# Performance work log

Measured on AMD Instinct MI355X. Metric: run time of the kernel, lower is better.

The kernel has to match this reference:

```python
import jax, jax.numpy as jnp
import numpy as np
import math

WINDOW = 14
NUM_HEADS = 12


def setup_inputs() -> dict:
    key = jax.random.key(0)
    k1, k2, k3 = jax.random.split(key, 3)
    B, H, W, C = 8, 80, 80, 768
    x = jax.random.normal(k1, (B, H * W, C), dtype=jnp.float32)
    Wqkv = jax.random.normal(k2, (C, 3 * C), dtype=jnp.float32) * 0.02
    Wproj = jax.random.normal(k3, (C, C), dtype=jnp.float32) * 0.02
    bproj = jnp.zeros((C,), dtype=jnp.float32)
    return {"x": x, "Wqkv": Wqkv, "Wproj": Wproj, "bproj": bproj, "H": H, "W": W}


def reference(x, Wqkv, Wproj, bproj, H, W):
    B, N, C = x.shape
    w = WINDOW
    nh = NUM_HEADS
    hd = C // nh
    scale = hd ** (-0.5)
    Hp = math.ceil(H / w) * w
    Wp = math.ceil(W / w) * w
    nH, nW = Hp // w, Wp // w
    L, Nw = nH * nW, w * w

    qkv = x @ Wqkv                                   # [B, N, 3C]
    grid = qkv.reshape(B, H, W, 3 * C)
    grid = jnp.pad(grid, ((0, 0), (0, Hp - H), (0, Wp - W), (0, 0)))
    # window partition: [B, nH, w, nW, w, 3C] -> [B, L, Nw, 3, nh, hd]
    win = grid.reshape(B, nH, w, nW, w, 3 * C).transpose(0, 1, 3, 2, 4, 5)
    win = win.reshape(B, L, Nw, 3, nh, hd)
    q = win[:, :, :, 0].transpose(0, 1, 3, 2, 4)     # [B, L, nh, Nw, hd]
    k = win[:, :, :, 1].transpose(0, 1, 3, 2, 4)
    v = win[:, :, :, 2].transpose(0, 1, 3, 2, 4)

    attn = jnp.einsum('blhnd,blhmd->blhnm', q, k) * scale
    attn = jax.nn.softmax(attn, axis=-1)
    out = jnp.einsum('blhnm,blhmd->blhnd', attn, v)  # [B, L, nh, Nw, hd]

    # window merge (fold with stride == kernel, non-overlapping)
    out = out.transpose(0, 1, 3, 2, 4).reshape(B, nH, nW, w, w, C)
    out = out.transpose(0, 1, 3, 2, 4, 5).reshape(B, Hp, Wp, C)
    out = out[:, :H, :W, :].reshape(B, N, C)
    return out @ Wproj + bproj
```

## Files before the change

kernel.cpp:

```cpp
#include <hip/hip_runtime.h>

typedef unsigned short u16;
typedef __attribute__((ext_vector_type(4))) float f32x4;
typedef __attribute__((ext_vector_type(8))) short bf16x8;

__device__ __forceinline__ u16 f2bf(float f) {
  unsigned u = __builtin_bit_cast(unsigned, f);
  u += 0x7FFFu + ((u >> 16) & 1u);
  return (u16)(u >> 16);
}

__device__ __forceinline__ void load16(const void* g, void* l) {
  __builtin_amdgcn_global_load_lds((const __attribute__((address_space(1))) void*)g,
                                   (__attribute__((address_space(3))) void*)l, 16, 0, 0);
}

#define LDS_ORDER() do { __builtin_amdgcn_s_waitcnt(0xC07F); asm volatile("" ::: "memory"); } while (0)

#define FENCE() asm volatile("" ::: "memory")
#define BARRIER() do { FENCE(); __builtin_amdgcn_s_barrier(); FENCE(); } while (0)
#define WAIT_VM2() asm volatile("s_waitcnt vmcnt(2)" ::: "memory")
#define WAIT_VM0() asm volatile("s_waitcnt vmcnt(0)" ::: "memory")
#define LGKM0() asm volatile("s_waitcnt lgkmcnt(0)" ::: "memory")


__global__ void cvt_x(const float* __restrict__ in, u16* __restrict__ out, int n4) {
  int i = blockIdx.x * 256 + threadIdx.x;
  if (i < n4) {
    float4 v = ((const float4*)in)[i];
    ushort4 o;
    o.x = f2bf(v.x); o.y = f2bf(v.y); o.z = f2bf(v.z); o.w = f2bf(v.w);
    ((ushort4*)out)[i] = o;
  }
}

__global__ void cvt_wt(const float* __restrict__ W, u16* __restrict__ Wt, int K, int N) {
  int idx = blockIdx.x * 256 + threadIdx.x;
  if (idx < N * K) {
    int n = idx / K, k = idx - n * K;
    Wt[idx] = f2bf(W[(size_t)k * N + n]);
  }
}


template <int MB, int NB>
__device__ __forceinline__ void mfma_quad(f32x4 (&acc)[8][4], const bf16x8 (&af)[4][2],
                                          const bf16x8 (&bf_)[4][2]) {
  __builtin_amdgcn_s_setprio(1);
#pragma unroll
  for (int mf = 0; mf < 4; mf++)
#pragma unroll
    for (int nf = 0; nf < 2; nf++) {
      acc[MB + mf][NB + nf] = __builtin_amdgcn_mfma_f32_16x16x32_bf16(
          af[mf][0], bf_[NB + nf][0], acc[MB + mf][NB + nf], 0, 0, 0);
      acc[MB + mf][NB + nf] = __builtin_amdgcn_mfma_f32_16x16x32_bf16(
          af[mf][1], bf_[NB + nf][1], acc[MB + mf][NB + nf], 0, 0, 0);
    }
  __builtin_amdgcn_s_setprio(0);
}

__device__ __forceinline__ void mm256_core(const u16* __restrict__ A,
                                           const u16* __restrict__ Bt,
                                           int bm, int bn,
                                           u16* lds, f32x4 (&acc)[8][4]) {
  const int K = 768;
  const int t = threadIdx.x;
  const int lane = t & 63, wave = t >> 6;
  const int wm = wave >> 2, wn = wave & 3;
  const int colq = lane & 15, quad = lane >> 4;

  const u16* Ab = A + (size_t)bm * 256 * K;
  const u16* Bb = Bt + (size_t)bn * 256 * K;

  u16* const lA = lds;
  u16* const lB = lds + 32768;

  const int srow = t >> 3;
  const int gslot = (t & 7) ^ (srow & 7);

#define STAGE_(gb, lb)                                                          \
  do {                                                                          \
    load16((gb) + (size_t)srow * K + gslot * 8, (lb) + t * 8);                  \
    load16((gb) + (size_t)(srow + 64) * K + gslot * 8, (lb) + (t + 512) * 8);   \
  } while (0)
#define STAGE_A(jj, h) STAGE_(Ab + (size_t)((h) * 128) * K + (jj) * 64, \
                              lA + ((jj) & 1) * 16384 + (h) * 8192)
#define STAGE_B(jj, h) STAGE_(Bb + (size_t)((h) * 128) * K + (jj) * 64, \
                              lB + ((jj) & 1) * 16384 + (h) * 8192)

  const int arow_lo = wm * 128 + colq;
  const int brow_lo = wn * 64 + colq;
  const int swz = (colq & 7) << 3;
#define RD(buf, row, kk) (*(const bf16x8*)&(buf)[(row) * 64 + (((kk) * 32 + quad * 8) ^ swz)])

  bf16x8 af[4][2], bf_[4][2];

  STAGE_A(0, 0); STAGE_A(0, 1); STAGE_B(0, 0); STAGE_B(0, 1);
  STAGE_A(1, 0);
  WAIT_VM2();
  BARRIER();

#pragma unroll 2
  for (int j = 0; j < 12; ++j) {
    const u16* cA = lA + (j & 1) * 16384;
    const u16* cB = lB + (j & 1) * 16384;

#pragma unroll
    for (int mf = 0; mf < 4; mf++) {
      af[mf][0] = RD(cA, arow_lo + mf * 16, 0);
      af[mf][1] = RD(cA, arow_lo + mf * 16, 1);
    }
#pragma unroll
    for (int nf = 0; nf < 2; nf++) {
      bf_[nf][0] = RD(cB, brow_lo + nf * 16, 0);
      bf_[nf][1] = RD(cB, brow_lo + nf * 16, 1);
    }
    if (j < 11) STAGE_A(j + 1, 1);
    BARRIER();
    mfma_quad<0, 0>(acc, af, bf_);
    LGKM0();
    BARRIER();

#pragma unroll
    for (int nf = 0; nf < 2; nf++) {
      bf_[2 + nf][0] = RD(cB, brow_lo + (2 + nf) * 16, 0);
      bf_[2 + nf][1] = RD(cB, brow_lo + (2 + nf) * 16, 1);
    }
    if (j < 11) STAGE_B(j + 1, 0);
    BARRIER();
    mfma_quad<0, 2>(acc, af, bf_);
    LGKM0();
    BARRIER();

#pragma unroll
    for (int mf = 0; mf < 4; mf++) {
      af[mf][0] = RD(cA, arow_lo + 64 + mf * 16, 0);
      af[mf][1] = RD(cA, arow_lo + 64 + mf * 16, 1);
    }
    if (j < 11) STAGE_B(j + 1, 1);
    BARRIER();
    mfma_quad<4, 0>(acc, af, bf_);
    LGKM0();
    BARRIER();

    if (j < 10) STAGE_A(j + 2, 0);
    BARRIER();
    mfma_quad<4, 2>(acc, af, bf_);
    if (j < 10) { WAIT_VM2(); }
    else if (j < 11) { WAIT_VM0(); }
    BARRIER();
  }
#undef RD
#undef STAGE_A
#undef STAGE_B
#undef STAGE_
}


__global__ __launch_bounds__(512, 2) void gemm_qkv(const u16* __restrict__ A,
                                                   const u16* __restrict__ Bt,
                                                   u16* __restrict__ qkvP) {
  __shared__ __align__(16) u16 lds[65536];
  const int nx = gridDim.x;
  const int nwg = nx * gridDim.y;
  const int bid = blockIdx.y * nx + blockIdx.x;
  const int cpx = nwg >> 3;
  const int sid = (bid & 7) * cpx + (bid >> 3);
  const int bm = sid / nx, bn = sid - bm * nx;

  f32x4 acc[8][4] = {};
  mm256_core(A, Bt, bm, bn, lds, acc);

  const int t = threadIdx.x;
  const int lane = t & 63, wave = t >> 6;
  const int wm = wave >> 2, wn = wave & 3;
  const int colq = lane & 15, quad = lane >> 4;

  const int c64 = bn * 4 + wn;
  const int mat = c64 / 12;
  const int hh = c64 - mat * 12;
  const int r0 = bm * 256 + wm * 128 + quad * 4;
#pragma unroll
  for (int mf = 0; mf < 8; mf++) {
#pragma unroll
    for (int r = 0; r < 4; r++) {
      int row = r0 + mf * 16 + r;
      int bb = row / 6400;
      int rem = row - bb * 6400;
      int y = rem / 80, x = rem - (rem / 80) * 80;
      int wy = y / 14, wx = x / 14;
      int iy = y - wy * 14, ix = x - wx * 14;
      int win = wy * 6 + wx;
      int kidx = iy * 14 + ix;
      size_t base = ((size_t)((bb * 36 + win) * 3 + mat) * 12 + hh) * 12544 + (size_t)kidx * 64;
#pragma unroll
      for (int nf = 0; nf < 4; nf++)
        qkvP[base + nf * 16 + colq] = f2bf(acc[mf][nf][r]);
    }
  }
}


__global__ __launch_bounds__(512, 2) void gemm_proj(const u16* __restrict__ A,
                                                    const u16* __restrict__ Bt,
                                                    float* __restrict__ C,
                                                    const float* __restrict__ bias) {
  __shared__ __align__(16) u16 lds[65536];
  const int nx = gridDim.x;
  const int nwg = nx * gridDim.y;
  const int bid = blockIdx.y * nx + blockIdx.x;
  const int cpx = nwg >> 3;
  const int sid = (bid & 7) * cpx + (bid >> 3);
  const int bm = sid / nx, bn = sid - bm * nx;

  f32x4 acc[8][4] = {};
  mm256_core(A, Bt, bm, bn, lds, acc);

  const int t = threadIdx.x;
  const int lane = t & 63, wave = t >> 6;
  const int wm = wave >> 2, wn = wave & 3;
  const int colq = lane & 15, quad = lane >> 4;

  const int r0 = bm * 256 + wm * 128 + quad * 4;
  const int c0 = bn * 256 + wn * 64 + colq;
  float bv[4];
#pragma unroll
  for (int nf = 0; nf < 4; nf++) bv[nf] = bias[c0 + nf * 16];
#pragma unroll
  for (int mf = 0; mf < 8; mf++)
#pragma unroll
    for (int nf = 0; nf < 4; nf++)
#pragma unroll
      for (int r = 0; r < 4; r++)
        C[(size_t)(r0 + mf * 16 + r) * 768 + (c0 + nf * 16)] = acc[mf][nf][r] + bv[nf];
}


__global__ __launch_bounds__(256) void win_attn(const u16* __restrict__ qkvP,
                                                u16* __restrict__ out) {
  __shared__ __align__(16) u16 sK[2 * 208 * 32];
  __shared__ __align__(16) u16 sVt[7 * 64 * 32];
  __shared__ __align__(16) u16 sVrow[200 * 64];

  const int h = blockIdx.x;
  const int win = blockIdx.y;
  const int b = blockIdx.z;
  const int wy = win / 6, wx = win - wy * 6;
  const int y0 = wy * 14, x0 = wx * 14;
  const int t = threadIdx.x, wave = t >> 6, lane = t & 63;
  const int colq = lane & 15, quad = lane >> 4;

  const size_t bwin = (size_t)(b * 36 + win) * 3;
  const u16* qbase = qkvP + ((bwin + 0) * 12 + h) * 12544;
  const u16* kbase = qkvP + ((bwin + 1) * 12 + h) * 12544;
  const u16* vbase = qkvP + ((bwin + 2) * 12 + h) * 12544;

  for (int s = t; s < 3264; s += 256) {
    if (s < 1664) {
      int half = s / 832;
      int rem = s - half * 832;
      int row = rem >> 2, e = rem & 3;
      int srow = row < 196 ? row : 0;
      load16(kbase + srow * 64 + half * 32 + e * 8, (u16*)sK + s * 8);
    } else {
      int s2 = s - 1664;
      load16(vbase + s2 * 8, sVrow + s2 * 8);
    }
  }
  __syncthreads();

  const bool boundary = (wx == 5) || (wy == 5);
  for (int jj = t; jj < 14336; jj += 256) {
    int kc = jj >> 11;
    int r2 = jj & 2047;
    int j = r2 >> 6, d = r2 & 63;
    int k = (j + d) & 31;
    int kidx = kc * 32 + k;
    u16 val = 0;
    if (kidx < 196) {
      int iy = kidx / 14, ix = kidx - (kidx / 14) * 14;
      if (y0 + iy < 80 && x0 + ix < 80) val = sVrow[kidx * 64 + d];
    }
    sVt[kc * 2048 + d * 32 + k] = val;
  }
  if (boundary) {
    for (int jj = t; jj < 13312; jj += 256) {
      int row = jj >> 6, d = jj & 63;
      if (row < 196) {
        int iy = row / 14, ix = row - (row / 14) * 14;
        if (y0 + iy >= 80 || x0 + ix >= 80)
          sK[((d >> 5) * 208 + row) * 32 + (d & 31)] = 0;
      }
    }
  }
  __syncthreads();

  u16* sPw = sVrow + wave * 640;

  int mt = wave;
  const u16* qp = qbase + (mt * 16 + colq) * 64 + quad * 8;
  bf16x8 qa0 = *(const bf16x8*)qp;
  bf16x8 qa1 = *(const bf16x8*)(qp + 32);
  while (mt < 13) {
    int mtn = mt + 4;
    bf16x8 qn0 = qa0, qn1 = qa1;
    if (mtn < 13) {
      const u16* qp2 = qbase + (mtn * 16 + colq) * 64 + quad * 8;
      qn0 = *(const bf16x8*)qp2;
      qn1 = *(const bf16x8*)(qp2 + 32);
    }

    f32x4 s[13];
#pragma unroll
    for (int nt = 0; nt < 13; nt++) {
      bf16x8 kb0 = *(const bf16x8*)&sK[(nt * 16 + colq) * 32 + quad * 8];
      bf16x8 kb1 = *(const bf16x8*)&sK[((208 + nt * 16 + colq)) * 32 + quad * 8];
      f32x4 a = {0.f, 0.f, 0.f, 0.f};
      a = __builtin_amdgcn_mfma_f32_16x16x32_bf16(qa0, kb0, a, 0, 0, 0);
      a = __builtin_amdgcn_mfma_f32_16x16x32_bf16(qa1, kb1, a, 0, 0, 0);
      s[nt] = a;
    }

    float mx[4] = {-1e30f, -1e30f, -1e30f, -1e30f};
#pragma unroll
    for (int nt = 0; nt < 13; nt++)
#pragma unroll
      for (int r = 0; r < 4; r++) {
        float v = s[nt][r] * 0.125f;
        if (nt == 12 && colq >= 4) v = -1e30f;
        s[nt][r] = v;
        mx[r] = fmaxf(mx[r], v);
      }
#pragma unroll
    for (int off = 1; off < 16; off <<= 1)
#pragma unroll
      for (int r = 0; r < 4; r++) mx[r] = fmaxf(mx[r], __shfl_xor(mx[r], off));
    float sm[4] = {0.f, 0.f, 0.f, 0.f};
#pragma unroll
    for (int nt = 0; nt < 13; nt++)
#pragma unroll
      for (int r = 0; r < 4; r++) {
        float e = __expf(s[nt][r] - mx[r]);
        s[nt][r] = e;
        sm[r] += e;
      }
#pragma unroll
    for (int off = 1; off < 16; off <<= 1)
#pragma unroll
      for (int r = 0; r < 4; r++) sm[r] += __shfl_xor(sm[r], off);
    float rs[4];
#pragma unroll
    for (int r = 0; r < 4; r++) rs[r] = 1.0f / sm[r];

    f32x4 o[4] = {};
#pragma unroll
    for (int kc = 0; kc < 7; kc++) {
      const int nt0 = kc * 2, nt1 = kc * 2 + 1;
#pragma unroll
      for (int r = 0; r < 4; r++) {
        sPw[(quad * 4 + r) * 36 + colq] = f2bf(s[nt0][r] * rs[r]);
        sPw[(quad * 4 + r) * 36 + 16 + colq] = (nt1 < 13) ? f2bf(s[nt1][r] * rs[r]) : (u16)0;
      }
      LDS_ORDER();
      bf16x8 pa = *(const bf16x8*)&sPw[colq * 36 + quad * 8];
#pragma unroll
      for (int dt = 0; dt < 4; dt++) {
        bf16x8 vb = *(const bf16x8*)&sVt[(kc * 64 + dt * 16 + colq) * 32 + quad * 8];
        o[dt] = __builtin_amdgcn_mfma_f32_16x16x32_bf16(pa, vb, o[dt], 0, 0, 0);
      }
      LDS_ORDER();
    }

#pragma unroll
    for (int r = 0; r < 4; r++) {
      int qr = mt * 16 + quad * 4 + r;
      if (qr < 196) {
        int iy = qr / 14, ix = qr - (qr / 14) * 14;
        int y = y0 + iy, x = x0 + ix;
        if (y < 80 && x < 80) {
          size_t off = ((size_t)(b * 6400 + y * 80 + x)) * 768 + h * 64 + colq;
#pragma unroll
          for (int dt = 0; dt < 4; dt++) out[off + dt * 16] = f2bf(o[dt][r]);
        }
      }
    }
    qa0 = qn0; qa1 = qn1;
    mt = mtn;
  }
}


extern "C" void kernel_launch(void* const* d_in, const int* in_sizes, int n_in,
                              void* d_out, int out_size, void* d_ws, size_t ws_size,
                              hipStream_t stream) {
  const float* x     = (const float*)d_in[0];
  const float* Wqkv  = (const float*)d_in[1];
  const float* Wproj = (const float*)d_in[2];
  const float* bproj = (const float*)d_in[3];

  char* ws = (char*)d_ws;
  const size_t QKVP_BYTES = (size_t)130056192 * 2 + 4096;
  const size_t X_BYTES    = (size_t)51200 * 768 * 2;
  const size_t WQT_BYTES  = (size_t)2304 * 768 * 2;
  u16* qkvP   = (u16*)ws;
  u16* xbf    = (u16*)(ws + QKVP_BYTES);
  u16* wqkvT  = (u16*)(ws + QKVP_BYTES + X_BYTES);
  u16* wprojT = (u16*)(ws + QKVP_BYTES + X_BYTES + WQT_BYTES);
  u16* aout   = xbf;

  cvt_x<<<38400, 256, 0, stream>>>(x, xbf, 9830400);
  cvt_wt<<<6912, 256, 0, stream>>>(Wqkv, wqkvT, 768, 2304);
  cvt_wt<<<2304, 256, 0, stream>>>(Wproj, wprojT, 768, 768);
  gemm_qkv<<<dim3(9, 200), 512, 0, stream>>>(xbf, wqkvT, qkvP);
  win_attn<<<dim3(12, 36, 8), 256, 0, stream>>>(qkvP, aout);
  gemm_proj<<<dim3(3, 200), 512, 0, stream>>>(aout, wprojT, (float*)d_out, bproj);
}
```

Measured before the change: 779.6 us.

## Keep softmax probabilities in registers and swizzle K/V LDS layouts in window attention

The window attention kernel now computes the score tile with K as the A operand, so each lane holds one query column. That lets the softmax reductions shrink to two cross-lane shuffles, and the normalised probabilities are packed straight into bf16 registers as the MFMA A operand, removing the per-chunk LDS round trip and its waits. K is loaded with an XOR swizzle, and V is transposed on load from global with byte permutes into a swizzled layout, replacing the staging buffer and second transpose pass. Zeroing of padded K/V rows moves into a separate pre-pass kernel on the workspace, and the kernel asks for 3 blocks per CU. The risks are the extra launch and the reliance on the QKV GEMM never overwriting the padded rows.

Result: faster. 749.2 us (-3.9%).

```diff
diff --git a/kernel.cpp b/kernel.cpp
--- a/kernel.cpp
+++ b/kernel.cpp
@@ -3,6 +3,12 @@
 typedef unsigned short u16;
 typedef __attribute__((ext_vector_type(4))) float f32x4;
 typedef __attribute__((ext_vector_type(8))) short bf16x8;
+typedef __attribute__((ext_vector_type(4))) short bf16x4;
+typedef __attribute__((ext_vector_type(2))) unsigned uint32x2;
+
+#ifndef __has_builtin
+#define __has_builtin(x) 0
+#endif
 
 __device__ __forceinline__ u16 f2bf(float f) {
   unsigned u = __builtin_bit_cast(unsigned, f);
@@ -15,7 +21,22 @@
                                    (__attribute__((address_space(3))) void*)l, 16, 0, 0);
 }
 
-#define LDS_ORDER() do { __builtin_amdgcn_s_waitcnt(0xC07F); asm volatile("" ::: "memory"); } while (0)
+__device__ __forceinline__ unsigned cvt_pk_bf16(float lo, float hi) {
+  unsigned r;
+  asm("v_cvt_pk_bf16_f32 %0, %1, %2" : "=v"(r) : "v"(lo), "v"(hi));
+  return r;
+}
+
+__device__ __forceinline__ f32x4 mfma16_bf16(bf16x4 a, bf16x4 b, f32x4 c) {
+#if __has_builtin(__builtin_amdgcn_mfma_f32_16x16x16bf16_1k)
+  return __builtin_amdgcn_mfma_f32_16x16x16bf16_1k(a, b, c, 0, 0, 0);
+#else
+  f32x4 d;
+  asm volatile("v_mfma_f32_16x16x16_bf16 %0, %1, %2, %3\n\ts_nop 7\n\ts_nop 3"
+               : "=&v"(d) : "v"(a), "v"(b), "v"(c));
+  return d;
+#endif
+}
 
 #define FENCE() asm volatile("" ::: "memory")
 #define BARRIER() do { FENCE(); __builtin_amdgcn_s_barrier(); FENCE(); } while (0)
@@ -40,6 +61,22 @@
     int n = idx / K, k = idx - n * K;
     Wt[idx] = f2bf(W[(size_t)k * N + n]);
   }
+}
+
+__global__ void zero_pad(u16* __restrict__ qkvP) {
+  int tid = blockIdx.x * 256 + threadIdx.x;
+  if (tid >= 1354752) return;
+  int kidx = tid % 196; int t2 = tid / 196;
+  int h = t2 % 12;      int t3 = t2 / 12;
+  int matp = t3 % 2;    int t4 = t3 / 2;
+  int win = t4 % 36;    int b = t4 / 36;
+  int wy = win / 6, wx = win - wy * 6;
+  int iy = kidx / 14, ix = kidx - iy * 14;
+  if (wy * 14 + iy < 80 && wx * 14 + ix < 80) return;
+  size_t base = ((size_t)((b * 36 + win) * 3 + (matp + 1)) * 12 + h) * 12544 + (size_t)kidx * 64;
+  f32x4 z = {};
+#pragma unroll
+  for (int i = 0; i < 8; i++) ((f32x4*)(qkvP + base))[i] = z;
 }
 
 
@@ -236,15 +273,12 @@
 }
 
 
-__global__ __launch_bounds__(256) void win_attn(const u16* __restrict__ qkvP,
-                                                u16* __restrict__ out) {
-  __shared__ __align__(16) u16 sK[2 * 208 * 32];
-  __shared__ __align__(16) u16 sVt[7 * 64 * 32];
-  __shared__ __align__(16) u16 sVrow[200 * 64];
-
-  const int h = blockIdx.x;
-  const int win = blockIdx.y;
-  const int b = blockIdx.z;
+__global__ __launch_bounds__(256, 3) void win_attn(const u16* __restrict__ qkvP,
+                                                   u16* __restrict__ out) {
+  __shared__ __align__(16) u16 sK[208 * 64];
+  __shared__ __align__(16) u16 sVt[13 * 1024];
+
+  const int h = blockIdx.x, win = blockIdx.y, b = blockIdx.z;
   const int wy = win / 6, wx = win - wy * 6;
   const int y0 = wy * 14, x0 = wx * 14;
   const int t = threadIdx.x, wave = t >> 6, lane = t & 63;
@@ -255,47 +289,39 @@
   const u16* kbase = qkvP + ((bwin + 1) * 12 + h) * 12544;
   const u16* vbase = qkvP + ((bwin + 2) * 12 + h) * 12544;
 
-  for (int s = t; s < 3264; s += 256) {
-    if (s < 1664) {
-      int half = s / 832;
-      int rem = s - half * 832;
-      int row = rem >> 2, e = rem & 3;
-      int srow = row < 196 ? row : 0;
-      load16(kbase + srow * 64 + half * 32 + e * 8, (u16*)sK + s * 8);
-    } else {
-      int s2 = s - 1664;
-      load16(vbase + s2 * 8, sVrow + s2 * 8);
+  for (int s = t; s < 1664; s += 256) {
+    int row = s >> 3, g = s & 7;
+    int srow = row < 196 ? row : 0;
+    load16(kbase + srow * 64 + ((g ^ (row & 7)) << 3), (u16*)sK + s * 8);
+  }
+
+  for (int u = t; u < 416; u += 256) {
+    int kq = u >> 3, dg = u & 7;
+    int nt = kq >> 2, q = kq & 3;
+    uint4 a0 = {}, a1 = {}, a2 = {}, a3 = {};
+    if (kq < 49) {
+      const uint4* vp = (const uint4*)(vbase + kq * 256 + dg * 8);
+      a0 = vp[0]; a1 = vp[8]; a2 = vp[16]; a3 = vp[24];
+    }
+    const unsigned* r0p = (const unsigned*)&a0;
+    const unsigned* r1p = (const unsigned*)&a1;
+    const unsigned* r2p = (const unsigned*)&a2;
+    const unsigned* r3p = (const unsigned*)&a3;
+#pragma unroll
+    for (int dd = 0; dd < 8; dd++) {
+      unsigned sel = (dd & 1) ? 0x07060302u : 0x05040100u;
+      unsigned lo = __builtin_amdgcn_perm(r1p[dd >> 1], r0p[dd >> 1], sel);
+      unsigned hi = __builtin_amdgcn_perm(r3p[dd >> 1], r2p[dd >> 1], sel);
+      int byteoff = nt * 2048 + (dg >> 1) * 512 + q * 128 +
+                    ((((dg & 1) * 8 + dd) ^ (q << 2)) << 3);
+      uint32x2 wv; wv[0] = lo; wv[1] = hi;
+      *(uint32x2*)((char*)sVt + byteoff) = wv;
     }
   }
   __syncthreads();
 
-  const bool boundary = (wx == 5) || (wy == 5);
-  for (int jj = t; jj < 14336; jj += 256) {
-    int kc = jj >> 11;
-    int r2 = jj & 2047;
-    int j = r2 >> 6, d = r2 & 63;
-    int k = (j + d) & 31;
-    int kidx = kc * 32 + k;
-    u16 val = 0;
-    if (kidx < 196) {
-      int iy = kidx / 14, ix = kidx - (kidx / 14) * 14;
-      if (y0 + iy < 80 && x0 + ix < 80) val = sVrow[kidx * 64 + d];
-    }
-    sVt[kc * 2048 + d * 32 + k] = val;
-  }
-  if (boundary) {
-    for (int jj = t; jj < 13312; jj += 256) {
-      int row = jj >> 6, d = jj & 63;
-      if (row < 196) {
-        int iy = row / 14, ix = row - (row / 14) * 14;
-        if (y0 + iy >= 80 || x0 + ix >= 80)
-          sK[((d >> 5) * 208 + row) * 32 + (d & 31)] = 0;
-      }
-    }
-  }
-  __syncthreads();
-
-  u16* sPw = sVrow + wave * 640;
+  const int kswz = (colq & 7) << 3;
+  const int vtoff = quad * 128 + ((colq ^ (quad << 2)) << 3);
 
   int mt = wave;
   const u16* qp = qbase + (mt * 16 + colq) * 64 + quad * 8;
@@ -311,65 +337,65 @@
     }
 
     f32x4 s[13];
+    __builtin_amdgcn_s_setprio(1);
 #pragma unroll
     for (int nt = 0; nt < 13; nt++) {
-      bf16x8 kb0 = *(const bf16x8*)&sK[(nt * 16 + colq) * 32 + quad * 8];
-      bf16x8 kb1 = *(const bf16x8*)&sK[((208 + nt * 16 + colq)) * 32 + quad * 8];
+      const u16* kr = &sK[(nt * 16 + colq) * 64];
+      bf16x8 kb0 = *(const bf16x8*)&kr[(quad * 8) ^ kswz];
+      bf16x8 kb1 = *(const bf16x8*)&kr[(32 + quad * 8) ^ kswz];
       f32x4 a = {0.f, 0.f, 0.f, 0.f};
-      a = __builtin_amdgcn_mfma_f32_16x16x32_bf16(qa0, kb0, a, 0, 0, 0);
-      a = __builtin_amdgcn_mfma_f32_16x16x32_bf16(qa1, kb1, a, 0, 0, 0);
+      a = __builtin_amdgcn_mfma_f32_16x16x32_bf16(kb0, qa0, a, 0, 0, 0);
+      a = __builtin_amdgcn_mfma_f32_16x16x32_bf16(kb1, qa1, a, 0, 0, 0);
       s[nt] = a;
     }
-
-    float mx[4] = {-1e30f, -1e30f, -1e30f, -1e30f};
+    __builtin_amdgcn_s_setprio(0);
+
+    float mx = -1e30f;
 #pragma unroll
     for (int nt = 0; nt < 13; nt++)
 #pragma unroll
       for (int r = 0; r < 4; r++) {
         float v = s[nt][r] * 0.125f;
-        if (nt == 12 && colq >= 4) v = -1e30f;
+        if (nt == 12 && quad != 0) v = -1e30f;
         s[nt][r] = v;
-        mx[r] = fmaxf(mx[r], v);
+        mx = fmaxf(mx, v);
       }
-#pragma unroll
-    for (int off = 1; off < 16; off <<= 1)
-#pragma unroll
-      for (int r = 0; r < 4; r++) mx[r] = fmaxf(mx[r], __shfl_xor(mx[r], off));
-    float sm[4] = {0.f, 0.f, 0.f, 0.f};
+    mx = fmaxf(mx, __shfl_xor(mx, 16));
+    mx = fmaxf(mx, __shfl_xor(mx, 32));
+    float sm = 0.f;
 #pragma unroll
     for (int nt = 0; nt < 13; nt++)
 #pragma unroll
       for (int r = 0; r < 4; r++) {
-        float e = __expf(s[nt][r] - mx[r]);
+        float e = __expf(s[nt][r] - mx);
         s[nt][r] = e;
-        sm[r] += e;
+        sm += e;
       }
-#pragma unroll
-    for (int off = 1; off < 16; off <<= 1)
-#pragma unroll
-      for (int r = 0; r < 4; r++) sm[r] += __shfl_xor(sm[r], off);
-    float rs[4];
-#pragma unroll
-    for (int r = 0; r < 4; r++) rs[r] = 1.0f / sm[r];
+    sm += __shfl_xor(sm, 16);
+    sm += __shfl_xor(sm, 32);
+    float rs = 1.0f / sm;
+
+    unsigned pk0[13], pk1[13];
+#pragma unroll
+    for (int nt = 0; nt < 13; nt++) {
+      pk0[nt] = cvt_pk_bf16(s[nt][0] * rs, s[nt][1] * rs);
+      pk1[nt] = cvt_pk_bf16(s[nt][2] * rs, s[nt][3] * rs);
+    }
 
     f32x4 o[4] = {};
-#pragma unroll
-    for (int kc = 0; kc < 7; kc++) {
-      const int nt0 = kc * 2, nt1 = kc * 2 + 1;
-#pragma unroll
-      for (int r = 0; r < 4; r++) {
-        sPw[(quad * 4 + r) * 36 + colq] = f2bf(s[nt0][r] * rs[r]);
-        sPw[(quad * 4 + r) * 36 + 16 + colq] = (nt1 < 13) ? f2bf(s[nt1][r] * rs[r]) : (u16)0;
+    __builtin_amdgcn_s_setprio(1);
+#pragma unroll
+    for (int nt = 0; nt < 13; nt++) {
+      uint32x2 pw; pw[0] = pk0[nt]; pw[1] = pk1[nt];
+      bf16x4 pa = __builtin_bit_cast(bf16x4, pw);
+      const char* vtb = (const char*)sVt + nt * 2048 + vtoff;
+#pragma unroll
+      for (int dt = 0; dt < 4; dt++) {
+        bf16x4 vb = *(const bf16x4*)(vtb + dt * 512);
+        o[dt] = mfma16_bf16(pa, vb, o[dt]);
       }
-      LDS_ORDER();
-      bf16x8 pa = *(const bf16x8*)&sPw[colq * 36 + quad * 8];
-#pragma unroll
-      for (int dt = 0; dt < 4; dt++) {
-        bf16x8 vb = *(const bf16x8*)&sVt[(kc * 64 + dt * 16 + colq) * 32 + quad * 8];
-        o[dt] = __builtin_amdgcn_mfma_f32_16x16x32_bf16(pa, vb, o[dt], 0, 0, 0);
-      }
-      LDS_ORDER();
-    }
+    }
+    __builtin_amdgcn_s_setprio(0);
 
 #pragma unroll
     for (int r = 0; r < 4; r++) {
@@ -411,6 +437,7 @@
   cvt_x<<<38400, 256, 0, stream>>>(x, xbf, 9830400);
   cvt_wt<<<6912, 256, 0, stream>>>(Wqkv, wqkvT, 768, 2304);
   cvt_wt<<<2304, 256, 0, stream>>>(Wproj, wprojT, 768, 768);
+  zero_pad<<<5292, 256, 0, stream>>>(qkvP);
   gemm_qkv<<<dim3(9, 200), 512, 0, stream>>>(xbf, wqkvT, qkvP);
   win_attn<<<dim3(12, 36, 8), 256, 0, stream>>>(qkvP, aout);
   gemm_proj<<<dim3(3, 200), 512, 0, stream>>>(aout, wprojT, (float*)d_out, bproj);
```
